# Performance work log

Measured on AMD Instinct MI355X. Metric: run time of the kernel, lower is better.

## Reference

```python
import jax, jax.numpy as jnp
import numpy as np

XYZ_MIN = np.array([-1.0, -1.0, -1.0], np.float32)
XYZ_MAX = np.array([1.0, 1.0, 1.0], np.float32)
N_SAMPLES = 256
T_NEAR, T_FAR = 0.05, 2.0
ALPHA_INIT = 1e-6
ACT_SHIFT = float(np.log(1.0 / (1.0 - ALPHA_INIT) - 1.0))  # density bias shift
INTERVAL = 0.5  # stepsize * voxel_size_ratio
VIEWBASE_PE = 4


def trilerp(grid, pts):
    """grid: [C, X, Y, Z]; pts: [P, 3] world coords. Returns [P, C]."""
    res = jnp.asarray(grid.shape[1:], dtype=pts.dtype)  # [3]
    ind = (pts - XYZ_MIN) / (XYZ_MAX - XYZ_MIN) * (res - 1.0)
    ind = jnp.clip(ind, 0.0, res - 1.0)
    i0 = jnp.minimum(jnp.floor(ind), res - 2.0).astype(jnp.int32)  # [P,3]
    f = ind - i0.astype(pts.dtype)  # [P,3] fractional offsets
    x0, y0, z0 = i0[:, 0], i0[:, 1], i0[:, 2]
    x1, y1, z1 = x0 + 1, y0 + 1, z0 + 1
    fx, fy, fz = f[:, 0], f[:, 1], f[:, 2]
    gx, gy, gz = 1.0 - fx, 1.0 - fy, 1.0 - fz
    out = (grid[:, x0, y0, z0] * (gx * gy * gz)
           + grid[:, x1, y0, z0] * (fx * gy * gz)
           + grid[:, x0, y1, z0] * (gx * fy * gz)
           + grid[:, x0, y0, z1] * (gx * gy * fz)
           + grid[:, x1, y1, z0] * (fx * fy * gz)
           + grid[:, x1, y0, z1] * (fx * gy * fz)
           + grid[:, x0, y1, z1] * (gx * fy * fz)
           + grid[:, x1, y1, z1] * (fx * fy * fz))  # [C,P]
    return out.T


def setup_inputs() -> dict:
    key = jax.random.key(0)
    ks = jax.random.split(key, 10)
    N = 4096
    rays_o = jax.random.normal(ks[0], (N, 3), jnp.float32) * 0.05
    rays_d = jax.random.normal(ks[1], (N, 3), jnp.float32)
    density = jax.random.normal(ks[2], (1, 1, 160, 160, 160), jnp.float32)
    k0 = jax.random.normal(ks[3], (1, 12, 160, 160, 160), jnp.float32) * 0.1
    w0 = jax.random.normal(ks[4], (39, 128), jnp.float32) * (1.0 / np.sqrt(39))
    b0 = jnp.zeros((128,), jnp.float32)
    w1 = jax.random.normal(ks[5], (128, 128), jnp.float32) * (1.0 / np.sqrt(128))
    b1 = jnp.zeros((128,), jnp.float32)
    w2 = jax.random.normal(ks[6], (128, 3), jnp.float32) * (1.0 / np.sqrt(128))
    b2 = jnp.zeros((3,), jnp.float32)
    return {"rays_o": rays_o, "rays_d": rays_d, "density": density, "k0": k0,
            "w0": w0, "b0": b0, "w1": w1, "b1": b1, "w2": w2, "b2": b2}


def reference(rays_o, rays_d, density, k0, w0, b0, w1, b1, w2, b2):
    N = rays_o.shape[0]
    dens_grid = density[0]            # [1,X,Y,Z]
    feat_grid = k0[0]                 # [C,X,Y,Z]
    viewdirs = rays_d / jnp.linalg.norm(rays_d, axis=-1, keepdims=True)
    t = jnp.linspace(T_NEAR, T_FAR, N_SAMPLES, dtype=rays_o.dtype)  # [S]
    pts = rays_o[:, None, :] + viewdirs[:, None, :] * t[None, :, None]  # [N,S,3]
    inbox = jnp.all((pts >= XYZ_MIN) & (pts <= XYZ_MAX), axis=-1)  # [N,S]
    flat = pts.reshape(-1, 3)

    # density -> alpha: 1 - (1 + exp(d + shift))^(-interval)   (Raw2Alpha)
    d = trilerp(dens_grid, flat)[:, 0].reshape(N, N_SAMPLES)
    alpha = 1.0 - jnp.power(1.0 + jnp.exp(d + ACT_SHIFT), -INTERVAL)
    alpha = jnp.where(inbox, alpha, 0.0)

    # alpha -> weights via exclusive transmittance cumprod (Alphas2Weights)
    T_full = jnp.cumprod(1.0 - alpha, axis=1)               # [N,S]
    T_excl = jnp.concatenate([jnp.ones((N, 1), alpha.dtype), T_full[:, :-1]], axis=1)
    weights = alpha * T_excl                                 # [N,S]
    alphainv_last = T_full[:, -1]                            # [N]

    # color features + view-direction positional encoding
    feat = trilerp(feat_grid, flat).reshape(N, N_SAMPLES, -1)  # [N,S,C]
    freqs = (2.0 ** jnp.arange(VIEWBASE_PE)).astype(rays_o.dtype)
    vf = viewdirs[:, :, None] * freqs[None, None, :]           # [N,3,PE]
    vemb = jnp.concatenate([viewdirs, jnp.sin(vf).reshape(N, -1), jnp.cos(vf).reshape(N, -1)], axis=-1)  # [N,27]
    x = jnp.concatenate([feat, jnp.broadcast_to(vemb[:, None, :], (N, N_SAMPLES, vemb.shape[-1]))], axis=-1)

    h = jax.nn.relu(x @ w0 + b0)
    h = jax.nn.relu(h @ w1 + b1)
    rgb = jax.nn.sigmoid(h @ w2 + b2)                          # [N,S,3]

    rgb_marched = jnp.einsum('ns,nsc->nc', weights, rgb) + alphainv_last[:, None] * 1.0  # white bg
    return rgb_marched
```

## Files before the change

kernel.cpp:

```cpp
#include <hip/hip_runtime.h>
#include <hip/hip_bf16.h>
#include <math.h>

#define ACT_SHIFT_F (-13.8155095579637744f)
#define GRID_VOX 4096000
#define GP_BYTES  (GRID_VOX * 32)
#define W0P_OFF   GP_BYTES
#define W1P_OFF   (W0P_OFF + 8 * 1024)
#define W2P_OFF   (W1P_OFF + 32 * 1024)
#define WS_NEED   ((size_t)(W2P_OFF + 4 * 1024))

typedef __bf16 bf16x8 __attribute__((ext_vector_type(8)));
typedef __bf16 bf16x2 __attribute__((ext_vector_type(2)));
typedef float  f32x4  __attribute__((ext_vector_type(4)));
typedef float  fv4    __attribute__((ext_vector_type(4)));

__device__ __forceinline__ float bfu(unsigned short b) {
    return __uint_as_float(((unsigned int)b) << 16);
}
__device__ __forceinline__ unsigned short f2bf(float x) {
    unsigned int u = __float_as_uint(x);
    u += 0x7fffu + ((u >> 16) & 1u);
    return (unsigned short)(u >> 16);
}
__device__ __forceinline__ void st_bf2(unsigned short* p, float lo, float hi) {
    bf16x2 v; v.x = (__bf16)lo; v.y = (__bf16)hi;
    *(bf16x2*)p = v;
}
__device__ __forceinline__ unsigned int packtr(float a, float b) {
    return (__float_as_uint(a) >> 16) | (__float_as_uint(b) & 0xffff0000u);
}
#define UNPK(u, lo, hi) { lo = __uint_as_float((u) << 16); hi = __uint_as_float((u) & 0xffff0000u); }

__global__ void repack_all(const float* __restrict__ dens, const float* __restrict__ k0,
                           const float* __restrict__ w0, const float* __restrict__ w1,
                           const float* __restrict__ w2,
                           unsigned short* __restrict__ gp, unsigned short* __restrict__ wp)
{
    const int b = blockIdx.x;
    if (b < 4000) {
        const int v4 = b * 1024 + threadIdx.x * 4;
        const fv4 d4 = __builtin_nontemporal_load((const fv4*)(dens + v4));
        fv4 c4[12];
        #pragma unroll
        for (int c = 0; c < 12; ++c)
            c4[c] = __builtin_nontemporal_load((const fv4*)(k0 + (size_t)c * GRID_VOX + v4));
        uint4* dst = (uint4*)(gp + (size_t)v4 * 16);
        #pragma unroll
        for (int j = 0; j < 4; ++j) {
            const float* cj = &((const float*)c4)[j];
            uint4 q0, q1;
            q0.x = packtr(d4[j],    cj[0]);
            q0.y = packtr(cj[4*1],  cj[4*2]);
            q0.z = packtr(cj[4*3],  cj[4*4]);
            q0.w = packtr(cj[4*5],  cj[4*6]);
            q1.x = packtr(cj[4*7],  cj[4*8]);
            q1.y = packtr(cj[4*9],  cj[4*10]);
            q1.z = packtr(cj[4*11], 0.f);
            q1.w = 0u;
            dst[j*2 + 0] = q0;
            dst[j*2 + 1] = q1;
        }
        return;
    }
    const int t = (b - 4000) * 256 + threadIdx.x;
    if (t >= 44 * 64) return;
    const int f = t >> 6, l = t & 63;
    const int n16 = l & 15, kg = l >> 4;
    unsigned short v[8];
    if (f < 8) {
        const int n = f * 16 + n16;
        #pragma unroll
        for (int j = 0; j < 8; ++j) {
            const int k = kg * 8 + j;
            v[j] = (k < 12) ? f2bf(w0[k * 128 + n]) : (unsigned short)0;
        }
    } else if (f < 40) {
        const int ff = f - 8, nt = ff >> 2, ks = ff & 3;
        const int n = nt * 16 + n16;
        #pragma unroll
        for (int j = 0; j < 8; ++j) {
            const int k = ks * 32 + kg * 8 + j;
            v[j] = f2bf(w1[k * 128 + n]);
        }
    } else {
        const int ks = f - 40;
        #pragma unroll
        for (int j = 0; j < 8; ++j) {
            const int k = ks * 32 + kg * 8 + j;
            v[j] = (n16 < 3) ? f2bf(w2[k * 3 + n16]) : (unsigned short)0;
        }
    }
    uint4 q;
    q.x = v[0] | (v[1] << 16); q.y = v[2] | (v[3] << 16);
    q.z = v[4] | (v[5] << 16); q.w = v[6] | (v[7] << 16);
    *(uint4*)(wp + f * 512 + l * 8) = q;
}

#define OFF_C0 0
#define OFF_C1 1
#define OFF_C2 160
#define OFF_C3 161
#define OFF_C4 25600
#define OFF_C5 25601
#define OFF_C6 25760
#define OFF_C7 25761

#define ISSUE_GATHER(CK) do {                                                        \
    const int s_ = (CK) * 128 + sl;                                                  \
    const float tp_ = 0.05f + (1.95f / 255.f) * (float)s_;                           \
    const float px_ = ox + vx*tp_, py_ = oy + vy*tp_, pz_ = oz + vz*tp_;             \
    inbox_p = (px_ >= -1.f) & (px_ <= 1.f) & (py_ >= -1.f) & (py_ <= 1.f) &          \
              (pz_ >= -1.f) & (pz_ <= 1.f);                                          \
    if (inbox_p) {                                                                   \
        const float ix_ = fminf(fmaxf((px_ + 1.f) * 79.5f, 0.f), 159.f);             \
        const float iy_ = fminf(fmaxf((py_ + 1.f) * 79.5f, 0.f), 159.f);             \
        const float iz_ = fminf(fmaxf((pz_ + 1.f) * 79.5f, 0.f), 159.f);             \
        const int x0_ = min((int)ix_, 158), y0_ = min((int)iy_, 158),                \
                  z0_ = min((int)iz_, 158);                                          \
        const size_t b_ = (size_t)((x0_ * 160 + y0_) * 160 + z0_) * 2 + hf;          \
        pq0 = gq[b_ + OFF_C0*2]; pq1 = gq[b_ + OFF_C1*2];                            \
        pq2 = gq[b_ + OFF_C2*2]; pq3 = gq[b_ + OFF_C3*2];                            \
        pq4 = gq[b_ + OFF_C4*2]; pq5 = gq[b_ + OFF_C5*2];                            \
        pq6 = gq[b_ + OFF_C6*2]; pq7 = gq[b_ + OFF_C7*2];                            \
    }                                                                                \
} while (0)

__global__ __launch_bounds__(256, 3)
void dvgo_mfma(const float* __restrict__ rays_o, const float* __restrict__ rays_d,
               const float* __restrict__ w0, const float* __restrict__ b0,
               const float* __restrict__ b1, const float* __restrict__ b2,
               const unsigned short* __restrict__ gp,
               const unsigned short* __restrict__ wpk,
               float* __restrict__ out)
{
    __shared__ unsigned short XH[128 * 136];
    __shared__ float shA[128];
    __shared__ float wts[128];
    __shared__ float b0eff[128];
    __shared__ float b1s[128];
    __shared__ float vemb[28];
    __shared__ float red[4][3];
    __shared__ float b2s[3];
    __shared__ float Tcs[3];
    __shared__ float spart;

    const int r = blockIdx.x, t = threadIdx.x;
    const int l = t & 63, wv = t >> 6;
    const int col = l & 15, rg = l >> 4;
    const int sl = t >> 1, hf = t & 1;

    const float ox = rays_o[r*3+0], oy = rays_o[r*3+1], oz = rays_o[r*3+2];
    const float dxr = rays_d[r*3+0], dyr = rays_d[r*3+1], dzr = rays_d[r*3+2];
    const float rn = rsqrtf(dxr*dxr + dyr*dyr + dzr*dzr);
    const float vx = dxr*rn, vy = dyr*rn, vz = dzr*rn;

    const uint4* gq = (const uint4*)gp;

    uint4 pq0, pq1, pq2, pq3, pq4, pq5, pq6, pq7;
    bool inbox_p = false;

    ISSUE_GATHER(0);

    if (t < 27) {
        float val;
        if (t < 3) val = (t == 0) ? vx : ((t == 1) ? vy : vz);
        else {
            int q = t - 3;
            const bool is_sin = q < 12;
            if (!is_sin) q -= 12;
            const int i = q >> 2, p = q & 3;
            const float a = ((i == 0) ? vx : ((i == 1) ? vy : vz)) * (float)(1 << p);
            val = is_sin ? sinf(a) : cosf(a);
        }
        vemb[t] = val;
    }
    if (t < 3)   b2s[t] = b2[t];
    if (t < 128) b1s[t] = b1[t];
    if (t == 0)  Tcs[0] = 1.f;
    __syncthreads();

    if (t < 128) {
        float a = b0[t];
        #pragma unroll
        for (int k = 0; k < 27; ++k) a = fmaf(vemb[k], w0[(12 + k) * 128 + t], a);
        b0eff[t] = a;
    }

    const unsigned short* w0p = wpk;
    const unsigned short* w1p = wpk + 8 * 512;
    const unsigned short* w2p = wpk + 40 * 512;

    float pacc = 0.f;

    #pragma unroll 1
    for (int ck = 0; ck < 2; ++ck) {
        {
            unsigned short* xrow = &XH[sl * 40];
            unsigned int*  xd   = (unsigned int*)xrow;
            if (inbox_p) {
                const int s = ck * 128 + sl;
                const float tp = 0.05f + (1.95f / 255.f) * (float)s;
                const float px = ox + vx*tp, py = oy + vy*tp, pz = oz + vz*tp;
                const float ix = fminf(fmaxf((px + 1.f) * 79.5f, 0.f), 159.f);
                const float iy = fminf(fmaxf((py + 1.f) * 79.5f, 0.f), 159.f);
                const float iz = fminf(fmaxf((pz + 1.f) * 79.5f, 0.f), 159.f);
                const int x0 = min((int)ix, 158), y0 = min((int)iy, 158), z0 = min((int)iz, 158);
                const float fx = ix - x0, fy = iy - y0, fz = iz - z0;
                const float gx = 1.f - fx, gy = 1.f - fy, gz = 1.f - fz;
                float w8[8];
                w8[0]=gx*gy*gz; w8[1]=gx*gy*fz; w8[2]=gx*fy*gz; w8[3]=gx*fy*fz;
                w8[4]=fx*gy*gz; w8[5]=fx*gy*fz; w8[6]=fx*fy*gz; w8[7]=fx*fy*fz;
                float a0=0,a1=0,a2=0,a3=0,a4=0,a5=0,a6=0,a7=0;
                #define CONSUME(Q, WI) {                                             \
                    float f0,f1,f2,f3,f4,f5,f6,f7;                                   \
                    UNPK((Q).x, f0, f1); UNPK((Q).y, f2, f3);                        \
                    UNPK((Q).z, f4, f5); UNPK((Q).w, f6, f7);                        \
                    const float wc = w8[WI];                                         \
                    a0=fmaf(wc,f0,a0); a1=fmaf(wc,f1,a1); a2=fmaf(wc,f2,a2);         \
                    a3=fmaf(wc,f3,a3); a4=fmaf(wc,f4,a4); a5=fmaf(wc,f5,a5);         \
                    a6=fmaf(wc,f6,a6); a7=fmaf(wc,f7,a7);                            \
                }
                CONSUME(pq0, 0); CONSUME(pq1, 1); CONSUME(pq2, 2); CONSUME(pq3, 3);
                CONSUME(pq4, 4); CONSUME(pq5, 5); CONSUME(pq6, 6); CONSUME(pq7, 7);
                #undef CONSUME
                if (hf == 0) {
                    st_bf2(&xrow[0], a1, a2);
                    st_bf2(&xrow[2], a3, a4);
                    st_bf2(&xrow[4], a5, a6);
                    *(__bf16*)&xrow[6] = (__bf16)a7;
                    const float e = expf(a0 + ACT_SHIFT_F);
                    const float op = 1.f + e;
                    const float alpha = e / (op + sqrtf(op));
                    wts[sl] = alpha;
                    shA[sl] = 1.f - alpha;
                } else {
                    *(__bf16*)&xrow[7] = (__bf16)a0;
                    st_bf2(&xrow[8],  a1, a2);
                    st_bf2(&xrow[10], a3, a4);
                }
            } else {
                if (hf == 0) {
                    xd[0]=0u; xd[1]=0u; xd[2]=0u; xrow[6]=0;
                    wts[sl] = 0.f;
                    shA[sl] = 1.f;
                } else {
                    xrow[7]=0; xd[4]=0u; xd[5]=0u;
                }
            }
            if (hf == 0) { xd[6]=0u; xd[7]=0u; xd[8]=0u; xd[9]=0u; xd[10]=0u; }
            else         { xd[11]=0u; xd[12]=0u; xd[13]=0u; xd[14]=0u; xd[15]=0u; }
            if (ck == 0) ISSUE_GATHER(1);
        }
        __syncthreads();

        const int row0 = wv * 32;

        bf16x8 A0[2];
        #pragma unroll
        for (int mt = 0; mt < 2; ++mt)
            A0[mt] = *(const bf16x8*)(&XH[(row0 + mt * 16 + col) * 40 + rg * 8]);

        float v = 1.f;
        if (t < 128) {
            v = shA[t];
            #pragma unroll
            for (int off = 1; off < 64; off <<= 1) {
                const float u = __shfl_up(v, off);
                if (l >= off) v *= u;
            }
            if (wv == 0 && l == 63) spart = v;
        }
        __syncthreads();
        if (t < 128) {
            float excl = __shfl_up(v, 1);
            if (l == 0) excl = 1.f;
            float E = Tcs[ck];
            const float sp = spart;
            if (wv == 1) E *= sp;
            const float w = wts[t] * E * excl;
            wts[t] = w;
            if (t == 127) Tcs[ck + 1] = Tcs[ck] * sp * v;
        }
        __syncthreads();

        {
            #pragma unroll 1
            for (int nt = 0; nt < 8; ++nt) {
                const bf16x8 B = *(const bf16x8*)(w0p + nt * 512 + l * 8);
                const float bias = b0eff[nt * 16 + col];
                #pragma unroll
                for (int mt = 0; mt < 2; ++mt) {
                    f32x4 acc = {0.f, 0.f, 0.f, 0.f};
                    acc = __builtin_amdgcn_mfma_f32_16x16x32_bf16(A0[mt], B, acc, 0, 0, 0);
                    #pragma unroll
                    for (int q = 0; q < 4; ++q) {
                        const float vv = fmaxf(acc[q] + bias, 0.f);
                        const float vo = __shfl_xor(vv, 1);
                        if ((l & 1) == 0) {
                            const int row = row0 + mt * 16 + rg * 4 + q;
                            st_bf2(&XH[row * 136 + nt * 16 + col], vv, vo);
                        }
                    }
                }
            }
        }

        {
            bf16x8 A1[2][4];
            #pragma unroll
            for (int mt = 0; mt < 2; ++mt)
                #pragma unroll
                for (int ks = 0; ks < 4; ++ks)
                    A1[mt][ks] = *(const bf16x8*)(&XH[(row0 + mt * 16 + col) * 136 + ks * 32 + rg * 8]);
            #pragma unroll 1
            for (int nt = 0; nt < 8; ++nt) {
                bf16x8 Bk[4];
                #pragma unroll
                for (int ks = 0; ks < 4; ++ks)
                    Bk[ks] = *(const bf16x8*)(w1p + (nt * 4 + ks) * 512 + l * 8);
                const float bias = b1s[nt * 16 + col];
                #pragma unroll
                for (int mt = 0; mt < 2; ++mt) {
                    f32x4 acc = {0.f, 0.f, 0.f, 0.f};
                    #pragma unroll
                    for (int ks = 0; ks < 4; ++ks)
                        acc = __builtin_amdgcn_mfma_f32_16x16x32_bf16(A1[mt][ks], Bk[ks], acc, 0, 0, 0);
                    #pragma unroll
                    for (int q = 0; q < 4; ++q) {
                        const float vv = fmaxf(acc[q] + bias, 0.f);
                        const float vo = __shfl_xor(vv, 1);
                        if ((l & 1) == 0) {
                            const int row = row0 + mt * 16 + rg * 4 + q;
                            st_bf2(&XH[row * 136 + nt * 16 + col], vv, vo);
                        }
                    }
                }
            }
        }

        {
            bf16x8 Bk[4];
            #pragma unroll
            for (int ks = 0; ks < 4; ++ks)
                Bk[ks] = *(const bf16x8*)(w2p + ks * 512 + l * 8);
            const float bias2 = (col < 3) ? b2s[col] : 0.f;
            #pragma unroll
            for (int mt = 0; mt < 2; ++mt) {
                bf16x8 A2[4];
                #pragma unroll
                for (int ks = 0; ks < 4; ++ks)
                    A2[ks] = *(const bf16x8*)(&XH[(row0 + mt * 16 + col) * 136 + ks * 32 + rg * 8]);
                f32x4 acc = {0.f, 0.f, 0.f, 0.f};
                #pragma unroll
                for (int ks = 0; ks < 4; ++ks)
                    acc = __builtin_amdgcn_mfma_f32_16x16x32_bf16(A2[ks], Bk[ks], acc, 0, 0, 0);
                #pragma unroll
                for (int q = 0; q < 4; ++q) {
                    const float rv = acc[q] + bias2;
                    const float sg = 1.f / (1.f + expf(-rv));
                    const int srow = row0 + mt * 16 + rg * 4 + q;
                    pacc = fmaf(wts[srow], sg, pacc);
                }
            }
        }
        __syncthreads();
    }

    pacc += __shfl_xor(pacc, 16);
    pacc += __shfl_xor(pacc, 32);
    if (rg == 0 && col < 3) red[wv][col] = pacc;
    __syncthreads();
    if (t < 3) out[r * 3 + t] = red[0][t] + red[1][t] + red[2][t] + red[3][t] + Tcs[2];
}

__global__ __launch_bounds__(256, 2)
void dvgo_render(const float* __restrict__ rays_o, const float* __restrict__ rays_d,
                 const float* __restrict__ dens, const float* __restrict__ k0,
                 const float* __restrict__ w0, const float* __restrict__ b0,
                 const float* __restrict__ w1, const float* __restrict__ b1,
                 const float* __restrict__ w2, const float* __restrict__ b2,
                 float* __restrict__ out)
{
    __shared__ float xs[256 * 40];
    __shared__ float sh[256];
    __shared__ float wts[256];
    __shared__ float h0s[2][128];
    __shared__ float red[2][2][3];
    __shared__ float rgbacc[6];
    __shared__ float ainv_sh;

    const int r = blockIdx.x, tid = threadIdx.x;
    {
        const int s = tid;
        const float ox = rays_o[r*3+0], oy = rays_o[r*3+1], oz = rays_o[r*3+2];
        const float dxr = rays_d[r*3+0], dyr = rays_d[r*3+1], dzr = rays_d[r*3+2];
        const float rn = rsqrtf(dxr*dxr + dyr*dyr + dzr*dzr);
        const float vx = dxr*rn, vy = dyr*rn, vz = dzr*rn;
        const float t = 0.05f + 1.95f * (1.0f/255.0f) * (float)s;
        const float px = ox + vx*t, py = oy + vy*t, pz = oz + vz*t;
        const bool inbox = (px >= -1.f) && (px <= 1.f) && (py >= -1.f) && (py <= 1.f) &&
                           (pz >= -1.f) && (pz <= 1.f);
        const float ix = fminf(fmaxf((px + 1.f) * 79.5f, 0.f), 159.f);
        const float iy = fminf(fmaxf((py + 1.f) * 79.5f, 0.f), 159.f);
        const float iz = fminf(fmaxf((pz + 1.f) * 79.5f, 0.f), 159.f);
        const int x0 = min((int)ix, 158), y0 = min((int)iy, 158), z0 = min((int)iz, 158);
        const float fx = ix - x0, fy = iy - y0, fz = iz - z0;
        const float gx = 1.f - fx, gy = 1.f - fy, gz = 1.f - fz;
        const int DX = 25600, DY = 160;
        const int base = (x0*160 + y0)*160 + z0;
        const float w000=gx*gy*gz, w100=fx*gy*gz, w010=gx*fy*gz, w001=gx*gy*fz;
        const float w110=fx*fy*gz, w101=fx*gy*fz, w011=gx*fy*fz, w111=fx*fy*fz;
        float alpha = 0.f;
        if (inbox) {
            const float d = dens[base]*w000 + dens[base+DX]*w100 + dens[base+DY]*w010 +
                            dens[base+1]*w001 + dens[base+DX+DY]*w110 + dens[base+DX+1]*w101 +
                            dens[base+DY+1]*w011 + dens[base+DX+DY+1]*w111;
            const float e = expf(d + ACT_SHIFT_F);
            const float op = 1.f + e;
            alpha = e / (op + sqrtf(op));
        }
        sh[s] = 1.f - alpha;
        __syncthreads();
        #pragma unroll
        for (int off = 1; off < 256; off <<= 1) {
            const float v = (s >= off) ? sh[s - off] : 1.f;
            __syncthreads();
            sh[s] *= v;
            __syncthreads();
        }
        wts[s] = alpha * ((s == 0) ? 1.f : sh[s-1]);
        if (s == 255) ainv_sh = sh[255];
        if (s < 6) rgbacc[s] = 0.f;
        float* xrow = &xs[s*40];
        if (inbox) {
            #pragma unroll
            for (int c = 0; c < 12; ++c) {
                const float* g = k0 + c*4096000 + base;
                xrow[c] = g[0]*w000 + g[DX]*w100 + g[DY]*w010 + g[1]*w001 +
                          g[DX+DY]*w110 + g[DX+1]*w101 + g[DY+1]*w011 + g[DX+DY+1]*w111;
            }
        } else {
            #pragma unroll
            for (int c = 0; c < 12; ++c) xrow[c] = 0.f;
        }
        xrow[12]=vx; xrow[13]=vy; xrow[14]=vz;
        const float v3[3] = {vx, vy, vz};
        #pragma unroll
        for (int i = 0; i < 3; ++i)
            #pragma unroll
            for (int p = 0; p < 4; ++p) {
                const float a = v3[i] * (float)(1 << p);
                xrow[15 + i*4 + p] = sinf(a);
                xrow[27 + i*4 + p] = cosf(a);
            }
        xrow[39] = 0.f;
    }
    __syncthreads();
    const int j = tid & 127, sb = tid >> 7;
    float w0c[40];
    #pragma unroll
    for (int k = 0; k < 39; ++k) w0c[k] = w0[k*128 + j];
    w0c[39] = 0.f;
    float w1c[128];
    #pragma unroll
    for (int k = 0; k < 128; ++k) w1c[k] = w1[k*128 + j];
    const float b0j = b0[j], b1j = b1[j];
    const float w2r0 = w2[j*3+0], w2r1 = w2[j*3+1], w2r2 = w2[j*3+2];
    const float b20 = b2[0], b21 = b2[1], b22 = b2[2];
    const int lane = tid & 63, halfw = (tid >> 6) & 1;
    for (int it = 0; it < 128; ++it) {
        const int s = it*2 + sb;
        const float4* xrow4 = (const float4*)(&xs[s*40]);
        float acc = b0j;
        #pragma unroll
        for (int q = 0; q < 10; ++q) {
            const float4 v = xrow4[q];
            acc = fmaf(v.x, w0c[q*4+0], acc); acc = fmaf(v.y, w0c[q*4+1], acc);
            acc = fmaf(v.z, w0c[q*4+2], acc); acc = fmaf(v.w, w0c[q*4+3], acc);
        }
        h0s[sb][j] = fmaxf(acc, 0.f);
        __syncthreads();
        float acc1 = b1j;
        const float4* h4 = (const float4*)(&h0s[sb][0]);
        #pragma unroll
        for (int q = 0; q < 32; ++q) {
            const float4 v = h4[q];
            acc1 = fmaf(v.x, w1c[q*4+0], acc1); acc1 = fmaf(v.y, w1c[q*4+1], acc1);
            acc1 = fmaf(v.z, w1c[q*4+2], acc1); acc1 = fmaf(v.w, w1c[q*4+3], acc1);
        }
        const float hv = fmaxf(acc1, 0.f);
        float p0 = hv*w2r0, p1 = hv*w2r1, p2 = hv*w2r2;
        #pragma unroll
        for (int off = 32; off > 0; off >>= 1) {
            p0 += __shfl_down(p0, off); p1 += __shfl_down(p1, off); p2 += __shfl_down(p2, off);
        }
        if (lane == 0) { red[sb][halfw][0]=p0; red[sb][halfw][1]=p1; red[sb][halfw][2]=p2; }
        __syncthreads();
        if (tid == sb*128) {
            const float r0 = red[sb][0][0]+red[sb][1][0]+b20;
            const float r1 = red[sb][0][1]+red[sb][1][1]+b21;
            const float r2 = red[sb][0][2]+red[sb][1][2]+b22;
            const float wgt = wts[s];
            rgbacc[sb*3+0] += wgt / (1.f + expf(-r0));
            rgbacc[sb*3+1] += wgt / (1.f + expf(-r1));
            rgbacc[sb*3+2] += wgt / (1.f + expf(-r2));
        }
    }
    __syncthreads();
    if (tid < 3) out[r*3 + tid] = rgbacc[tid] + rgbacc[3 + tid] + ainv_sh;
}

extern "C" void kernel_launch(void* const* d_in, const int* in_sizes, int n_in,
                              void* d_out, int out_size, void* d_ws, size_t ws_size,
                              hipStream_t stream)
{
    const float* rays_o = (const float*)d_in[0];
    const float* rays_d = (const float*)d_in[1];
    const float* dens   = (const float*)d_in[2];
    const float* k0     = (const float*)d_in[3];
    const float* w0     = (const float*)d_in[4];
    const float* b0     = (const float*)d_in[5];
    const float* w1     = (const float*)d_in[6];
    const float* b1     = (const float*)d_in[7];
    const float* w2     = (const float*)d_in[8];
    const float* b2     = (const float*)d_in[9];
    float* out = (float*)d_out;
    const int N = in_sizes[0] / 3;

    if (ws_size >= WS_NEED) {
        unsigned short* gp  = (unsigned short*)d_ws;
        unsigned short* wpk = (unsigned short*)((char*)d_ws + W0P_OFF);
        repack_all<<<dim3(4011), dim3(256), 0, stream>>>(dens, k0, w0, w1, w2, gp, wpk);
        dvgo_mfma<<<dim3(N), dim3(256), 0, stream>>>(rays_o, rays_d, w0, b0, b1, b2,
                                                     gp, wpk, out);
    } else {
        dvgo_render<<<dim3(N), dim3(256), 0, stream>>>(rays_o, rays_d, dens, k0,
                                                       w0, b0, w1, b1, w2, b2, out);
    }
}
```

Before: 487.8 us.

## Switch grid and MLP to fp16 with packed-half trilinear interpolation and prefetched weights

Repacks the voxel grid and MLP weights as fp16 instead of bf16, and does the trilinear accumulation with packed half2 multiply-adds rather than unpacking to fp32 FMAs. The MLP now uses f16 MFMA instructions, initializes accumulators with the bias, writes single halves instead of shuffling pairs, and double-buffers the weight fragment loads across n-tiles. It also moves a block barrier so layers 0 and 1 run without an intermediate sync. The aim is to cut ALU work in the gather and interpolation stage and to reduce latency stalls in the MLP. In exchange, fp16 accumulation of the density channel before the exponential loses precision, and the range of intermediate activations is narrower than with bf16.

After: 457.5 us. 6.2% less time.

```diff
diff --git a/kernel.cpp b/kernel.cpp
--- a/kernel.cpp
+++ b/kernel.cpp
@@ -10,27 +10,18 @@
 #define W2P_OFF   (W1P_OFF + 32 * 1024)
 #define WS_NEED   ((size_t)(W2P_OFF + 4 * 1024))
 
-typedef __bf16 bf16x8 __attribute__((ext_vector_type(8)));
-typedef __bf16 bf16x2 __attribute__((ext_vector_type(2)));
-typedef float  f32x4  __attribute__((ext_vector_type(4)));
-typedef float  fv4    __attribute__((ext_vector_type(4)));
-
-__device__ __forceinline__ float bfu(unsigned short b) {
-    return __uint_as_float(((unsigned int)b) << 16);
+typedef _Float16 f16x8 __attribute__((ext_vector_type(8)));
+typedef _Float16 h2    __attribute__((ext_vector_type(2)));
+typedef float    f32x4 __attribute__((ext_vector_type(4)));
+typedef float    fv4   __attribute__((ext_vector_type(4)));
+
+__device__ __forceinline__ unsigned int pkh2(float a, float b) {
+    h2 v; v.x = (_Float16)a; v.y = (_Float16)b;
+    return __builtin_bit_cast(unsigned int, v);
 }
-__device__ __forceinline__ unsigned short f2bf(float x) {
-    unsigned int u = __float_as_uint(x);
-    u += 0x7fffu + ((u >> 16) & 1u);
-    return (unsigned short)(u >> 16);
+__device__ __forceinline__ unsigned short f2h(float x) {
+    _Float16 h = (_Float16)x; return __builtin_bit_cast(unsigned short, h);
 }
-__device__ __forceinline__ void st_bf2(unsigned short* p, float lo, float hi) {
-    bf16x2 v; v.x = (__bf16)lo; v.y = (__bf16)hi;
-    *(bf16x2*)p = v;
-}
-__device__ __forceinline__ unsigned int packtr(float a, float b) {
-    return (__float_as_uint(a) >> 16) | (__float_as_uint(b) & 0xffff0000u);
-}
-#define UNPK(u, lo, hi) { lo = __uint_as_float((u) << 16); hi = __uint_as_float((u) & 0xffff0000u); }
 
 __global__ void repack_all(const float* __restrict__ dens, const float* __restrict__ k0,
                            const float* __restrict__ w0, const float* __restrict__ w1,
@@ -50,14 +41,14 @@
         for (int j = 0; j < 4; ++j) {
             const float* cj = &((const float*)c4)[j];
             uint4 q0, q1;
-            q0.x = packtr(d4[j],    cj[0]);
-            q0.y = packtr(cj[4*1],  cj[4*2]);
-            q0.z = packtr(cj[4*3],  cj[4*4]);
-            q0.w = packtr(cj[4*5],  cj[4*6]);
-            q1.x = packtr(cj[4*7],  cj[4*8]);
-            q1.y = packtr(cj[4*9],  cj[4*10]);
-            q1.z = packtr(cj[4*11], 0.f);
-            q1.w = 0u;
+            q0.x = pkh2(cj[4*0],  cj[4*1]);
+            q0.y = pkh2(cj[4*2],  cj[4*3]);
+            q0.z = pkh2(cj[4*4],  cj[4*5]);
+            q0.w = pkh2(cj[4*6],  cj[4*7]);
+            q1.x = pkh2(cj[4*8],  cj[4*9]);
+            q1.y = pkh2(cj[4*10], cj[4*11]);
+            q1.z = 0u;
+            q1.w = pkh2(0.f, d4[j]);
             dst[j*2 + 0] = q0;
             dst[j*2 + 1] = q1;
         }
@@ -73,7 +64,7 @@
         #pragma unroll
         for (int j = 0; j < 8; ++j) {
             const int k = kg * 8 + j;
-            v[j] = (k < 12) ? f2bf(w0[k * 128 + n]) : (unsigned short)0;
+            v[j] = (k < 12) ? f2h(w0[k * 128 + n]) : (unsigned short)0;
         }
     } else if (f < 40) {
         const int ff = f - 8, nt = ff >> 2, ks = ff & 3;
@@ -81,14 +72,14 @@
         #pragma unroll
         for (int j = 0; j < 8; ++j) {
             const int k = ks * 32 + kg * 8 + j;
-            v[j] = f2bf(w1[k * 128 + n]);
+            v[j] = f2h(w1[k * 128 + n]);
         }
     } else {
         const int ks = f - 40;
         #pragma unroll
         for (int j = 0; j < 8; ++j) {
             const int k = ks * 32 + kg * 8 + j;
-            v[j] = (n16 < 3) ? f2bf(w2[k * 3 + n16]) : (unsigned short)0;
+            v[j] = (n16 < 3) ? f2h(w2[k * 3 + n16]) : (unsigned short)0;
         }
     }
     uint4 q;
@@ -156,6 +147,7 @@
     const float vx = dxr*rn, vy = dyr*rn, vz = dzr*rn;
 
     const uint4* gq = (const uint4*)gp;
+    _Float16* XHh = (_Float16*)XH;
 
     uint4 pq0, pq1, pq2, pq3, pq4, pq5, pq6, pq7;
     bool inbox_p = false;
@@ -196,8 +188,7 @@
     #pragma unroll 1
     for (int ck = 0; ck < 2; ++ck) {
         {
-            unsigned short* xrow = &XH[sl * 40];
-            unsigned int*  xd   = (unsigned int*)xrow;
+            unsigned int* xd = (unsigned int*)&XH[sl * 40];
             if (inbox_p) {
                 const int s = ck * 128 + sl;
                 const float tp = 0.05f + (1.95f / 255.f) * (float)s;
@@ -211,55 +202,55 @@
                 float w8[8];
                 w8[0]=gx*gy*gz; w8[1]=gx*gy*fz; w8[2]=gx*fy*gz; w8[3]=gx*fy*fz;
                 w8[4]=fx*gy*gz; w8[5]=fx*gy*fz; w8[6]=fx*fy*gz; w8[7]=fx*fy*fz;
-                float a0=0,a1=0,a2=0,a3=0,a4=0,a5=0,a6=0,a7=0;
+                h2 ah0 = {0, 0}, ah1 = {0, 0}, ah2 = {0, 0}, ah3 = {0, 0};
                 #define CONSUME(Q, WI) {                                             \
-                    float f0,f1,f2,f3,f4,f5,f6,f7;                                   \
-                    UNPK((Q).x, f0, f1); UNPK((Q).y, f2, f3);                        \
-                    UNPK((Q).z, f4, f5); UNPK((Q).w, f6, f7);                        \
-                    const float wc = w8[WI];                                         \
-                    a0=fmaf(wc,f0,a0); a1=fmaf(wc,f1,a1); a2=fmaf(wc,f2,a2);         \
-                    a3=fmaf(wc,f3,a3); a4=fmaf(wc,f4,a4); a5=fmaf(wc,f5,a5);         \
-                    a6=fmaf(wc,f6,a6); a7=fmaf(wc,f7,a7);                            \
+                    h2 wc2; wc2.x = (_Float16)w8[WI]; wc2.y = wc2.x;                 \
+                    ah0 += __builtin_bit_cast(h2, (Q).x) * wc2;                      \
+                    ah1 += __builtin_bit_cast(h2, (Q).y) * wc2;                      \
+                    ah2 += __builtin_bit_cast(h2, (Q).z) * wc2;                      \
+                    ah3 += __builtin_bit_cast(h2, (Q).w) * wc2;                      \
                 }
                 CONSUME(pq0, 0); CONSUME(pq1, 1); CONSUME(pq2, 2); CONSUME(pq3, 3);
                 CONSUME(pq4, 4); CONSUME(pq5, 5); CONSUME(pq6, 6); CONSUME(pq7, 7);
                 #undef CONSUME
                 if (hf == 0) {
-                    st_bf2(&xrow[0], a1, a2);
-                    st_bf2(&xrow[2], a3, a4);
-                    st_bf2(&xrow[4], a5, a6);
-                    *(__bf16*)&xrow[6] = (__bf16)a7;
-                    const float e = expf(a0 + ACT_SHIFT_F);
+                    xd[0] = __builtin_bit_cast(unsigned int, ah0);
+                    xd[1] = __builtin_bit_cast(unsigned int, ah1);
+                    xd[2] = __builtin_bit_cast(unsigned int, ah2);
+                    xd[3] = __builtin_bit_cast(unsigned int, ah3);
+                } else {
+                    xd[4] = __builtin_bit_cast(unsigned int, ah0);
+                    xd[5] = __builtin_bit_cast(unsigned int, ah1);
+                    xd[6] = 0u;
+                    xd[7] = 0u;
+                    const float dv = (float)ah3.y;
+                    const float e = expf(dv + ACT_SHIFT_F);
                     const float op = 1.f + e;
                     const float alpha = e / (op + sqrtf(op));
                     wts[sl] = alpha;
                     shA[sl] = 1.f - alpha;
-                } else {
-                    *(__bf16*)&xrow[7] = (__bf16)a0;
-                    st_bf2(&xrow[8],  a1, a2);
-                    st_bf2(&xrow[10], a3, a4);
                 }
             } else {
                 if (hf == 0) {
-                    xd[0]=0u; xd[1]=0u; xd[2]=0u; xrow[6]=0;
+                    xd[0]=0u; xd[1]=0u; xd[2]=0u; xd[3]=0u;
+                } else {
+                    xd[4]=0u; xd[5]=0u; xd[6]=0u; xd[7]=0u;
                     wts[sl] = 0.f;
                     shA[sl] = 1.f;
-                } else {
-                    xrow[7]=0; xd[4]=0u; xd[5]=0u;
                 }
             }
-            if (hf == 0) { xd[6]=0u; xd[7]=0u; xd[8]=0u; xd[9]=0u; xd[10]=0u; }
-            else         { xd[11]=0u; xd[12]=0u; xd[13]=0u; xd[14]=0u; xd[15]=0u; }
+            if (hf == 0) { xd[8]=0u;  xd[9]=0u;  xd[10]=0u; xd[11]=0u; }
+            else         { xd[12]=0u; xd[13]=0u; xd[14]=0u; xd[15]=0u; }
             if (ck == 0) ISSUE_GATHER(1);
         }
         __syncthreads();
 
         const int row0 = wv * 32;
 
-        bf16x8 A0[2];
+        f16x8 A0[2];
         #pragma unroll
         for (int mt = 0; mt < 2; ++mt)
-            A0[mt] = *(const bf16x8*)(&XH[(row0 + mt * 16 + col) * 40 + rg * 8]);
+            A0[mt] = *(const f16x8*)(&XH[(row0 + mt * 16 + col) * 40 + rg * 8]);
 
         float v = 1.f;
         if (t < 128) {
@@ -282,83 +273,98 @@
             wts[t] = w;
             if (t == 127) Tcs[ck + 1] = Tcs[ck] * sp * v;
         }
-        __syncthreads();
 
         {
+            #define L0_STEP(B, NT) {                                                  \
+                const float bias = b0eff[(NT) * 16 + col];                            \
+                _Pragma("unroll")                                                     \
+                for (int mt = 0; mt < 2; ++mt) {                                      \
+                    f32x4 acc = {bias, bias, bias, bias};                             \
+                    acc = __builtin_amdgcn_mfma_f32_16x16x32_f16(A0[mt], B, acc, 0, 0, 0); \
+                    _Pragma("unroll")                                                 \
+                    for (int q = 0; q < 4; ++q) {                                     \
+                        const float vv = fmaxf(acc[q], 0.f);                          \
+                        const int row = row0 + mt * 16 + rg * 4 + q;                  \
+                        XHh[row * 136 + (NT) * 16 + col] = (_Float16)vv;              \
+                    }                                                                 \
+                }                                                                     \
+            }
+            f16x8 Ba = *(const f16x8*)(w0p + l * 8);
             #pragma unroll 1
-            for (int nt = 0; nt < 8; ++nt) {
-                const bf16x8 B = *(const bf16x8*)(w0p + nt * 512 + l * 8);
-                const float bias = b0eff[nt * 16 + col];
-                #pragma unroll
-                for (int mt = 0; mt < 2; ++mt) {
-                    f32x4 acc = {0.f, 0.f, 0.f, 0.f};
-                    acc = __builtin_amdgcn_mfma_f32_16x16x32_bf16(A0[mt], B, acc, 0, 0, 0);
-                    #pragma unroll
-                    for (int q = 0; q < 4; ++q) {
-                        const float vv = fmaxf(acc[q] + bias, 0.f);
-                        const float vo = __shfl_xor(vv, 1);
-                        if ((l & 1) == 0) {
-                            const int row = row0 + mt * 16 + rg * 4 + q;
-                            st_bf2(&XH[row * 136 + nt * 16 + col], vv, vo);
-                        }
-                    }
-                }
-            }
-        }
+            for (int nt = 0; nt < 8; nt += 2) {
+                const f16x8 Bb = *(const f16x8*)(w0p + (nt + 1) * 512 + l * 8);
+                L0_STEP(Ba, nt);
+                if (nt < 6) Ba = *(const f16x8*)(w0p + (nt + 2) * 512 + l * 8);
+                L0_STEP(Bb, nt + 1);
+            }
+            #undef L0_STEP
+        }
+
+        f16x8 W2k[4];
+        #pragma unroll
+        for (int ks = 0; ks < 4; ++ks)
+            W2k[ks] = *(const f16x8*)(w2p + ks * 512 + l * 8);
 
         {
-            bf16x8 A1[2][4];
+            f16x8 A1[2][4];
             #pragma unroll
             for (int mt = 0; mt < 2; ++mt)
                 #pragma unroll
                 for (int ks = 0; ks < 4; ++ks)
-                    A1[mt][ks] = *(const bf16x8*)(&XH[(row0 + mt * 16 + col) * 136 + ks * 32 + rg * 8]);
+                    A1[mt][ks] = *(const f16x8*)(&XH[(row0 + mt * 16 + col) * 136 + ks * 32 + rg * 8]);
+            #define L1_STEP(BK, NT) {                                                 \
+                const float bias = b1s[(NT) * 16 + col];                              \
+                _Pragma("unroll")                                                     \
+                for (int mt = 0; mt < 2; ++mt) {                                      \
+                    f32x4 acc = {bias, bias, bias, bias};                             \
+                    _Pragma("unroll")                                                 \
+                    for (int ks = 0; ks < 4; ++ks)                                    \
+                        acc = __builtin_amdgcn_mfma_f32_16x16x32_f16(A1[mt][ks], BK[ks], acc, 0, 0, 0); \
+                    _Pragma("unroll")                                                 \
+                    for (int q = 0; q < 4; ++q) {                                     \
+                        const float vv = fmaxf(acc[q], 0.f);                          \
+                        const int row = row0 + mt * 16 + rg * 4 + q;                  \
+                        XHh[row * 136 + (NT) * 16 + col] = (_Float16)vv;              \
+                    }                                                                 \
+                }                                                                     \
+            }
+            f16x8 BkA[4], BkB[4];
+            #pragma unroll
+            for (int ks = 0; ks < 4; ++ks)
+                BkA[ks] = *(const f16x8*)(w1p + ks * 512 + l * 8);
             #pragma unroll 1
-            for (int nt = 0; nt < 8; ++nt) {
-                bf16x8 Bk[4];
+            for (int nt = 0; nt < 8; nt += 2) {
                 #pragma unroll
                 for (int ks = 0; ks < 4; ++ks)
-                    Bk[ks] = *(const bf16x8*)(w1p + (nt * 4 + ks) * 512 + l * 8);
-                const float bias = b1s[nt * 16 + col];
-                #pragma unroll
-                for (int mt = 0; mt < 2; ++mt) {
-                    f32x4 acc = {0.f, 0.f, 0.f, 0.f};
+                    BkB[ks] = *(const f16x8*)(w1p + ((nt + 1) * 4 + ks) * 512 + l * 8);
+                L1_STEP(BkA, nt);
+                if (nt < 6) {
                     #pragma unroll
                     for (int ks = 0; ks < 4; ++ks)
-                        acc = __builtin_amdgcn_mfma_f32_16x16x32_bf16(A1[mt][ks], Bk[ks], acc, 0, 0, 0);
-                    #pragma unroll
-                    for (int q = 0; q < 4; ++q) {
-                        const float vv = fmaxf(acc[q] + bias, 0.f);
-                        const float vo = __shfl_xor(vv, 1);
-                        if ((l & 1) == 0) {
-                            const int row = row0 + mt * 16 + rg * 4 + q;
-                            st_bf2(&XH[row * 136 + nt * 16 + col], vv, vo);
-                        }
-                    }
+                        BkA[ks] = *(const f16x8*)(w1p + ((nt + 2) * 4 + ks) * 512 + l * 8);
                 }
-            }
-        }
+                L1_STEP(BkB, nt + 1);
+            }
+            #undef L1_STEP
+        }
+
+        __syncthreads();
 
         {
-            bf16x8 Bk[4];
-            #pragma unroll
-            for (int ks = 0; ks < 4; ++ks)
-                Bk[ks] = *(const bf16x8*)(w2p + ks * 512 + l * 8);
             const float bias2 = (col < 3) ? b2s[col] : 0.f;
             #pragma unroll
             for (int mt = 0; mt < 2; ++mt) {
-                bf16x8 A2[4];
+                f16x8 A2[4];
                 #pragma unroll
                 for (int ks = 0; ks < 4; ++ks)
-                    A2[ks] = *(const bf16x8*)(&XH[(row0 + mt * 16 + col) * 136 + ks * 32 + rg * 8]);
-                f32x4 acc = {0.f, 0.f, 0.f, 0.f};
+                    A2[ks] = *(const f16x8*)(&XH[(row0 + mt * 16 + col) * 136 + ks * 32 + rg * 8]);
+                f32x4 acc = {bias2, bias2, bias2, bias2};
                 #pragma unroll
                 for (int ks = 0; ks < 4; ++ks)
-                    acc = __builtin_amdgcn_mfma_f32_16x16x32_bf16(A2[ks], Bk[ks], acc, 0, 0, 0);
+                    acc = __builtin_amdgcn_mfma_f32_16x16x32_f16(A2[ks], W2k[ks], acc, 0, 0, 0);
                 #pragma unroll
                 for (int q = 0; q < 4; ++q) {
-                    const float rv = acc[q] + bias2;
-                    const float sg = 1.f / (1.f + expf(-rv));
+                    const float sg = 1.f / (1.f + expf(-acc[q]));
                     const int srow = row0 + mt * 16 + rg * 4 + q;
                     pacc = fmaf(wts[srow], sg, pacc);
                 }
```
